# Kernel tuning notes

Hardware: AMD Instinct MI355X
Metric: run time of the kernel (lower is better)

The kernel has to match this reference:

```python
import jax, jax.numpy as jnp
import numpy as np

EPS = 1e-12  # F.normalize default eps


def _l2_normalize(x):
    # F.normalize(x, p=2) normalizes over dim=1 (channels) by default
    n = jnp.sqrt(jnp.sum(x * x, axis=1, keepdims=True))
    return x / jnp.maximum(n, EPS)


def _cost_volume(left, right, num_disp):
    # left, right: (N, C, H, W)
    l = _l2_normalize(left)
    r = _l2_normalize(right)
    # dot[n,h,x,y] = sum_c l[n,c,h,x] * r[n,c,h,y]   -> (N, H, W, W)
    dot = jnp.einsum('nchx,nchy->nhxy', l, r)
    W = left.shape[-1]
    x = jnp.arange(W)                                   # (W,)
    j = jnp.arange(num_disp)                            # (D,)
    # torch.diagonal(offset=-j) + F.pad((j,0)) picks dot[..., x, x-j] with zeros for x<j
    idx = jnp.clip(x[None, :] - j[:, None], 0, W - 1)   # (D, W)
    g = dot[:, :, x[None, :], idx]                      # (N, H, D, W)
    valid = (x[None, :] >= j[:, None])                  # (D, W)
    g = jnp.where(valid[None, None, :, :], g, jnp.zeros((), dtype=g.dtype))
    return jnp.transpose(g, (0, 2, 1, 3))               # (N, D, H, W)


def setup_inputs() -> dict:
    key = jax.random.key(0)
    ks = jax.random.split(key, 6)
    shapes = [(2, 32, 256, 512), (2, 64, 128, 256), (2, 96, 64, 128)]
    inp = {}
    for i, s in enumerate(shapes):
        inp[f'left{i}'] = jax.random.normal(ks[2 * i], s, dtype=jnp.float32)
        inp[f'right{i}'] = jax.random.normal(ks[2 * i + 1], s, dtype=jnp.float32)
    inp['max_disparity'] = 128
    return inp


def reference(left0, right0, left1, right1, left2, right2, max_disparity):
    lefts = [left0, left1, left2]
    rights = [right0, right1, right2]
    md = min(int(max_disparity), lefts[0].shape[-1])
    cost_volumes = []
    for i, (l, r) in enumerate(zip(lefts, rights)):
        cost_volumes.append(_cost_volume(l, r, md // (2 ** i)))
    return tuple(cost_volumes)
```

## Files before the change

kernel.cpp:

```cpp
#include <hip/hip_runtime.h>

typedef __attribute__((ext_vector_type(8))) short bf16x8;
typedef __attribute__((ext_vector_type(4))) float f32x4;

static __device__ __forceinline__ unsigned short f32_to_bf16(float f) {
    unsigned int x = __float_as_uint(f);
    x += 0x7fffu + ((x >> 16) & 1u);
    return (unsigned short)(x >> 16);
}

template<int C, int H, int W, int D, int TX, int NT>
__global__ __launch_bounds__(NT)
void cost_volume_mfma(const float* __restrict__ Lp, const float* __restrict__ Rp,
                      float* __restrict__ out)
{
    constexpr int RS = TX + D;
    constexpr int AS = C + 8;
    constexpr int KC = C / 32;
    constexpr int NW = NT / 64;
    static_assert(NW == TX / 16, "one wave per 16-wide x-tile");
    static_assert((AS * 2) % 16 == 0, "frag rows must be 16B aligned");

    constexpr int STAGE_F = C * (TX + RS);
    constexpr int OBUF_F  = D * TX;
    constexpr int UNION_F = STAGE_F > OBUF_F ? STAGE_F : OBUF_F;

    __shared__ __align__(16) float uni[UNION_F];
    __shared__ __align__(16) unsigned short Abf[RS * AS];
    __shared__ __align__(16) unsigned short Bbf[TX * AS];

    float* lsf  = uni;
    float* rsf  = uni + C * TX;
    float* obuf = uni;

    const int tid = threadIdx.x;
    constexpr int NXB = W / TX;
    const int bx = blockIdx.x;
    const int xb = bx % NXB;
    const int h  = (bx / NXB) % H;
    const int n  = bx / (NXB * H);
    const int X0 = xb * TX;

    for (int i = tid; i < C * TX / 4; i += NT) {
        const int c = i / (TX / 4), v = i % (TX / 4);
        *(float4*)&lsf[c * TX + 4 * v] =
            *(const float4*)&Lp[(((size_t)n * C + c) * H + h) * W + X0 + 4 * v];
    }
    for (int i = tid; i < C * RS / 4; i += NT) {
        const int c = i / (RS / 4), v = i % (RS / 4);
        const int y = X0 - D + 4 * v;
        const float* src = &Rp[(((size_t)n * C + c) * H + h) * W];
        float4 val;
        if (y >= 0) val = *(const float4*)&src[y];
        else {
            val.x = (y + 0) >= 0 ? src[y + 0] : 0.f;
            val.y = (y + 1) >= 0 ? src[y + 1] : 0.f;
            val.z = (y + 2) >= 0 ? src[y + 2] : 0.f;
            val.w = (y + 3) >= 0 ? src[y + 3] : 0.f;
        }
        *(float4*)&rsf[c * RS + 4 * v] = val;
    }
    __syncthreads();

    for (int col = tid; col < TX + RS; col += NT) {
        const float* src; int stride; unsigned short* dst;
        if (col < TX) { src = lsf + col;        stride = TX; dst = Bbf + col * AS; }
        else          { src = rsf + (col - TX); stride = RS; dst = Abf + (col - TX) * AS; }
        float v[C];
        float s = 0.f;
        #pragma unroll
        for (int c = 0; c < C; ++c) { v[c] = src[c * stride]; s += v[c] * v[c]; }
        const float inv = 1.0f / fmaxf(sqrtf(s), 1e-12f);
        #pragma unroll
        for (int c0 = 0; c0 < C; c0 += 8) {
            union { unsigned short us[8]; uint4 q; } p;
            #pragma unroll
            for (int k = 0; k < 8; ++k) p.us[k] = f32_to_bf16(v[c0 + k] * inv);
            *(uint4*)&dst[c0] = p.q;
        }
    }
    __syncthreads();

    const int wave = tid >> 6, lane = tid & 63;
    const int colc = lane & 15, quad = lane >> 4;

    bf16x8 bfr[KC];
    #pragma unroll
    for (int kc = 0; kc < KC; ++kc)
        bfr[kc] = *(const bf16x8*)&Bbf[(wave * 16 + colc) * AS + kc * 32 + quad * 8];

    const int xl = wave * 16 + colc;
    #pragma unroll
    for (int t = 0; t <= D / 16; ++t) {
        const int yt = wave + t;
        f32x4 acc = {0.f, 0.f, 0.f, 0.f};
        #pragma unroll
        for (int kc = 0; kc < KC; ++kc) {
            const bf16x8 a =
                *(const bf16x8*)&Abf[(yt * 16 + colc) * AS + kc * 32 + quad * 8];
            acc = __builtin_amdgcn_mfma_f32_16x16x32_bf16(a, bfr[kc], acc, 0, 0, 0);
        }
        const int jb = D + xl - yt * 16 - quad * 4;
        #pragma unroll
        for (int r = 0; r < 4; ++r) {
            const int j = jb - r;
            if (j >= 0 && j < D) obuf[j * TX + xl] = acc[r];
        }
    }
    __syncthreads();

    constexpr int JV = TX / 4;
    for (int i = tid; i < D * TX / 4; i += NT) {
        const int j = i / JV, c4 = i % JV;
        *(float4*)&out[(((size_t)n * D + j) * H + h) * W + X0 + 4 * c4] =
            *(const float4*)&obuf[j * TX + 4 * c4];
    }
}

extern "C" void kernel_launch(void* const* d_in, const int* in_sizes, int n_in,
                              void* d_out, int out_size, void* d_ws, size_t ws_size,
                              hipStream_t stream) {
    (void)in_sizes; (void)n_in; (void)d_ws; (void)ws_size; (void)out_size;
    const float* l0 = (const float*)d_in[0];
    const float* r0 = (const float*)d_in[1];
    const float* l1 = (const float*)d_in[2];
    const float* r1 = (const float*)d_in[3];
    const float* l2 = (const float*)d_in[4];
    const float* r2 = (const float*)d_in[5];

    float* o0 = (float*)d_out;
    float* o1 = o0 + (size_t)2 * 128 * 256 * 512;
    float* o2 = o1 + (size_t)2 * 64 * 128 * 256;

    cost_volume_mfma<32, 256, 512, 128, 64, 256>
        <<<2 * 256 * (512 / 64), 256, 0, stream>>>(l0, r0, o0);
    cost_volume_mfma<64, 128, 256, 64, 32, 128>
        <<<2 * 128 * (256 / 32), 128, 0, stream>>>(l1, r1, o1);
    cost_volume_mfma<96, 64, 128, 32, 32, 128>
        <<<2 * 64 * (128 / 32), 128, 0, stream>>>(l2, r2, o2);
}
```

Before: 312.2 us.

## Fuse three pyramid-level launches into one kernel with shared LDS pool

Replaces three separate kernel launches with a single launch that dispatches each block to a level by block index, sharing one statically sized LDS pool. Smaller levels now use 256 threads, with the extra waves splitting the disparity tiles among themselves. The output staging buffer is padded to reduce LDS bank conflicts, and normalization re-reads LDS instead of holding all channels in registers to cut register pressure. The single pool is sized for the largest level, which may reduce occupancy for the smaller levels.

New measurement: 318.5 us. 1.02x slower.

```diff
diff --git a/kernel.cpp b/kernel.cpp
--- a/kernel.cpp
+++ b/kernel.cpp
@@ -10,32 +10,30 @@
 }
 
 template<int C, int H, int W, int D, int TX, int NT>
-__global__ __launch_bounds__(NT)
-void cost_volume_mfma(const float* __restrict__ Lp, const float* __restrict__ Rp,
-                      float* __restrict__ out)
+__device__ __forceinline__ void level_body(char* pool, int bx,
+    const float* __restrict__ Lp, const float* __restrict__ Rp,
+    float* __restrict__ out)
 {
     constexpr int RS = TX + D;
     constexpr int AS = C + 8;
     constexpr int KC = C / 32;
-    constexpr int NW = NT / 64;
-    static_assert(NW == TX / 16, "one wave per 16-wide x-tile");
-    static_assert((AS * 2) % 16 == 0, "frag rows must be 16B aligned");
+    constexpr int NSTRIP = TX / 16;
+    constexpr int NSUB = (NT / 64) / NSTRIP;
+    constexpr int OST = TX + 4;
+    constexpr int STAGE_F = C * (TX + RS);
+    constexpr int OBUF_F  = D * OST;
+    constexpr int UNI_F   = STAGE_F > OBUF_F ? STAGE_F : OBUF_F;
+    static_assert((RS * AS * 2) % 16 == 0, "Bbf alignment");
 
-    constexpr int STAGE_F = C * (TX + RS);
-    constexpr int OBUF_F  = D * TX;
-    constexpr int UNION_F = STAGE_F > OBUF_F ? STAGE_F : OBUF_F;
-
-    __shared__ __align__(16) float uni[UNION_F];
-    __shared__ __align__(16) unsigned short Abf[RS * AS];
-    __shared__ __align__(16) unsigned short Bbf[TX * AS];
-
+    float* uni = (float*)pool;
+    unsigned short* Abf = (unsigned short*)(pool + ((UNI_F * 4 + 15) & ~15));
+    unsigned short* Bbf = Abf + RS * AS;
     float* lsf  = uni;
     float* rsf  = uni + C * TX;
     float* obuf = uni;
 
     const int tid = threadIdx.x;
     constexpr int NXB = W / TX;
-    const int bx = blockIdx.x;
     const int xb = bx % NXB;
     const int h  = (bx / NXB) % H;
     const int n  = bx / (NXB * H);
@@ -66,33 +64,35 @@
         const float* src; int stride; unsigned short* dst;
         if (col < TX) { src = lsf + col;        stride = TX; dst = Bbf + col * AS; }
         else          { src = rsf + (col - TX); stride = RS; dst = Abf + (col - TX) * AS; }
-        float v[C];
         float s = 0.f;
-        #pragma unroll
-        for (int c = 0; c < C; ++c) { v[c] = src[c * stride]; s += v[c] * v[c]; }
+        #pragma unroll 8
+        for (int c = 0; c < C; ++c) { const float v = src[c * stride]; s += v * v; }
         const float inv = 1.0f / fmaxf(sqrtf(s), 1e-12f);
         #pragma unroll
         for (int c0 = 0; c0 < C; c0 += 8) {
             union { unsigned short us[8]; uint4 q; } p;
             #pragma unroll
-            for (int k = 0; k < 8; ++k) p.us[k] = f32_to_bf16(v[c0 + k] * inv);
+            for (int k = 0; k < 8; ++k)
+                p.us[k] = f32_to_bf16(src[(c0 + k) * stride] * inv);
             *(uint4*)&dst[c0] = p.q;
         }
     }
     __syncthreads();
 
     const int wave = tid >> 6, lane = tid & 63;
+    const int strip = wave % NSTRIP;
+    const int sub   = wave / NSTRIP;
     const int colc = lane & 15, quad = lane >> 4;
 
     bf16x8 bfr[KC];
     #pragma unroll
     for (int kc = 0; kc < KC; ++kc)
-        bfr[kc] = *(const bf16x8*)&Bbf[(wave * 16 + colc) * AS + kc * 32 + quad * 8];
+        bfr[kc] = *(const bf16x8*)&Bbf[(strip * 16 + colc) * AS + kc * 32 + quad * 8];
 
-    const int xl = wave * 16 + colc;
+    const int xl = strip * 16 + colc;
     #pragma unroll
-    for (int t = 0; t <= D / 16; ++t) {
-        const int yt = wave + t;
+    for (int t = sub; t <= D / 16; t += NSUB) {
+        const int yt = strip + t;
         f32x4 acc = {0.f, 0.f, 0.f, 0.f};
         #pragma unroll
         for (int kc = 0; kc < KC; ++kc) {
@@ -104,7 +104,7 @@
         #pragma unroll
         for (int r = 0; r < 4; ++r) {
             const int j = jb - r;
-            if (j >= 0 && j < D) obuf[j * TX + xl] = acc[r];
+            if (j >= 0 && j < D) obuf[j * OST + xl] = acc[r];
         }
     }
     __syncthreads();
@@ -113,7 +113,27 @@
     for (int i = tid; i < D * TX / 4; i += NT) {
         const int j = i / JV, c4 = i % JV;
         *(float4*)&out[(((size_t)n * D + j) * H + h) * W + X0 + 4 * c4] =
-            *(const float4*)&obuf[j * TX + 4 * c4];
+            *(const float4*)&obuf[j * OST + 4 * c4];
+    }
+}
+
+#define POOL_BYTES 56832
+
+__global__ __launch_bounds__(256)
+void cost_volume_all(const float* __restrict__ l0, const float* __restrict__ r0,
+                     const float* __restrict__ l1, const float* __restrict__ r1,
+                     const float* __restrict__ l2, const float* __restrict__ r2,
+                     float* __restrict__ o0, float* __restrict__ o1,
+                     float* __restrict__ o2)
+{
+    __shared__ __align__(16) char pool[POOL_BYTES];
+    const int bx = blockIdx.x;
+    if (bx < 4096) {
+        level_body<32, 256, 512, 128, 64, 256>(pool, bx, l0, r0, o0);
+    } else if (bx < 4096 + 2048) {
+        level_body<64, 128, 256, 64, 32, 256>(pool, bx - 4096, l1, r1, o1);
+    } else {
+        level_body<96, 64, 128, 32, 32, 256>(pool, bx - 6144, l2, r2, o2);
     }
 }
 
@@ -132,10 +152,6 @@
     float* o1 = o0 + (size_t)2 * 128 * 256 * 512;
     float* o2 = o1 + (size_t)2 * 64 * 128 * 256;
 
-    cost_volume_mfma<32, 256, 512, 128, 64, 256>
-        <<<2 * 256 * (512 / 64), 256, 0, stream>>>(l0, r0, o0);
-    cost_volume_mfma<64, 128, 256, 64, 32, 128>
-        <<<2 * 128 * (256 / 32), 128, 0, stream>>>(l1, r1, o1);
-    cost_volume_mfma<96, 64, 128, 32, 32, 128>
-        <<<2 * 64 * (128 / 32), 128, 0, stream>>>(l2, r2, o2);
+    cost_volume_all<<<4096 + 2048 + 512, 256, 0, stream>>>(
+        l0, r0, l1, r1, l2, r2, o0, o1, o2);
 }
```
